# Kernel tuning notes

Measured on AMD Instinct MI355X. Metric: run time of the kernel, lower is better.

Reference implementation:

```python
import jax, jax.numpy as jnp
import numpy as np

BATCH, NSTEPS, IN_F, OUT_F = 8192, 16, 256, 512


def setup_inputs() -> dict:
    key = jax.random.key(0)
    ks = jax.random.split(key, 20)
    r = jax.random.normal
    return {
        "x": r(ks[0], (BATCH, NSTEPS, IN_F), jnp.float32),
        "C": r(ks[1], (BATCH, OUT_F, 1), jnp.float32),
        "H": r(ks[2], (BATCH, OUT_F, 1), jnp.float32),
        "fg_w_c": r(ks[3], (OUT_F, 1), jnp.float32),
        "fg_w_h": r(ks[4], (OUT_F, OUT_F), jnp.float32),
        "fg_w_x": r(ks[5], (OUT_F, IN_F), jnp.float32),
        "fg_b": r(ks[6], (OUT_F, 1), jnp.float32),
        "ig_w_c": r(ks[7], (OUT_F, 1), jnp.float32),
        "ig_w_h": r(ks[8], (OUT_F, OUT_F), jnp.float32),
        "ig_w_x": r(ks[9], (OUT_F, IN_F), jnp.float32),
        "ig_b": r(ks[10], (OUT_F, 1), jnp.float32),
        "in_w_h": r(ks[11], (OUT_F, OUT_F), jnp.float32),
        "in_w_x": r(ks[12], (OUT_F, IN_F), jnp.float32),
        "in_b": r(ks[13], (OUT_F, 1), jnp.float32),
        "og_w_cn": r(ks[14], (OUT_F, 1), jnp.float32),
        "og_w_h": r(ks[15], (OUT_F, OUT_F), jnp.float32),
        "og_w_x": r(ks[16], (OUT_F, IN_F), jnp.float32),
        "og_b": r(ks[17], (OUT_F, 1), jnp.float32),
        "n": 3,
    }


def reference(x, C, H,
              fg_w_c, fg_w_h, fg_w_x, fg_b,
              ig_w_c, ig_w_h, ig_w_x, ig_b,
              in_w_h, in_w_x, in_b,
              og_w_cn, og_w_h, og_w_x, og_b,
              n):
    # x: [B, T, IN] -> current step [B, IN, 1]
    x_cur = x[:, n, :, None]
    # peephole LSTM gates; matmul broadcasts [O,O] @ [B,O,1] -> [B,O,1]
    fg = jax.nn.sigmoid(fg_w_c * C + jnp.matmul(fg_w_h, H) + jnp.matmul(fg_w_x, x_cur) + fg_b)
    ig = jax.nn.sigmoid(ig_w_c * C + jnp.matmul(ig_w_h, H) + jnp.matmul(ig_w_x, x_cur) + ig_b)
    inn = jnp.tanh(jnp.matmul(in_w_h, H) + jnp.matmul(in_w_x, x_cur) + in_b)
    cm = fg * C + ig * inn
    og = jax.nn.sigmoid(og_w_cn * cm + jnp.matmul(og_w_h, H) + jnp.matmul(og_w_x, x_cur) + og_b)
    h = og * jnp.tanh(cm)
    return (cm, h)
```

## Files before the change

### kernel.cpp

```cpp
#include <hip/hip_runtime.h>


typedef _Float16 half8 __attribute__((ext_vector_type(8)));
typedef _Float16 half4v __attribute__((ext_vector_type(4)));
typedef float floatx4 __attribute__((ext_vector_type(4)));

#define BATCH 8192
#define NSTEPS 16
#define IN_F 256
#define OUT_F 512
#define KDIM 768
#define NDIM 2048
#define HSIZE ((size_t)BATCH * OUT_F)

#define BM 128
#define BN 128
#define BK 64

__device__ __forceinline__ void async_copy16(const void* gptr, void* lptr) {
  __builtin_amdgcn_global_load_lds(
      (const __attribute__((address_space(1))) unsigned int*)gptr,
      (__attribute__((address_space(3))) unsigned int*)lptr,
      16, 0, 0);
}

__device__ __forceinline__ float sigmoidf_(float x) {
  return 1.0f / (1.0f + __expf(-x));
}

__device__ __forceinline__ float tanhf_(float x) {
  x = fminf(fmaxf(x, -20.0f), 20.0f);
  float e = __expf(2.0f * x);
  return (e - 1.0f) / (e + 1.0f);
}

__global__ void pack_AW(const float* __restrict__ H, const float* __restrict__ x,
                        const int* __restrict__ nptr,
                        const float* __restrict__ fg_w_h, const float* __restrict__ fg_w_x,
                        const float* __restrict__ ig_w_h, const float* __restrict__ ig_w_x,
                        const float* __restrict__ in_w_h, const float* __restrict__ in_w_x,
                        const float* __restrict__ og_w_h, const float* __restrict__ og_w_x,
                        _Float16* __restrict__ A, _Float16* __restrict__ W) {
  const int blk = blockIdx.x;
  const int k = threadIdx.x * 4;
  const float* src;
  _Float16* dst;
  if (blk < BATCH) {
    const int b = blk;
    if (k < OUT_F) {
      src = H + (size_t)b * OUT_F + k;
    } else {
      const int n = *nptr;
      src = x + ((size_t)b * NSTEPS + n) * IN_F + (k - OUT_F);
    }
    dst = A + (size_t)b * KDIM + k;
  } else {
    const int row = blk - BATCH;
    const int g  = (row >> 4) & 3;
    const int jj = ((row >> 6) << 4) | (row & 15);
    if (k < OUT_F) {
      const float* wh = (g == 0) ? fg_w_h : (g == 1) ? ig_w_h : (g == 2) ? in_w_h : og_w_h;
      src = wh + (size_t)jj * OUT_F + k;
    } else {
      const float* wx = (g == 0) ? fg_w_x : (g == 1) ? ig_w_x : (g == 2) ? in_w_x : og_w_x;
      src = wx + (size_t)jj * IN_F + (k - OUT_F);
    }
    dst = W + (size_t)row * KDIM + k;
  }
  float4 v = *(const float4*)src;
  half4v h = {(_Float16)v.x, (_Float16)v.y, (_Float16)v.z, (_Float16)v.w};
  *(half4v*)dst = h;
}

__global__ __launch_bounds__(256, 4) void gemm_lstm(
    const _Float16* __restrict__ A, const _Float16* __restrict__ W,
    const float* __restrict__ C,
    const float* __restrict__ fg_w_c, const float* __restrict__ fg_b,
    const float* __restrict__ ig_w_c, const float* __restrict__ ig_b,
    const float* __restrict__ in_b,
    const float* __restrict__ og_w_cn, const float* __restrict__ og_b,
    float* __restrict__ out) {
  __shared__ __align__(16) _Float16 As[BM * BK];
  __shared__ __align__(16) _Float16 Bs[BN * BK];

  const int tid = threadIdx.x;
  const int lane = tid & 63;
  const int wave = tid >> 6;
  const int quad = lane >> 4;
  const int l16 = lane & 15;
  const int m0 = blockIdx.y * BM;
  const int n0 = blockIdx.x * BN;
  const int mw = (wave >> 1) * 64;
  const int nw = (wave & 1) * 64;

  const int jj = (((n0 + nw) >> 6) << 4) | l16;
  const float fwc = fg_w_c[jj], fb = fg_b[jj];
  const float iwc = ig_w_c[jj], ib = ig_b[jj];
  const float nb  = in_b[jj];
  const float owc = og_w_cn[jj], ob = og_b[jj];

  floatx4 acc[4][4] = {};

  for (int kt = 0; kt < KDIM; kt += BK) {
    __syncthreads();
#pragma unroll
    for (int r = 0; r < 4; ++r) {
      const int g = r * 256 + tid;
      const int row = g >> 3;
      const int cl = g & 7;
      const int cg = cl ^ (row & 7);
      async_copy16(A + (size_t)(m0 + row) * KDIM + kt + cg * 8,
                   (_Float16*)As + g * 8);
      async_copy16(W + (size_t)(n0 + row) * KDIM + kt + cg * 8,
                   (_Float16*)Bs + g * 8);
    }
    __syncthreads();

#pragma unroll
    for (int ks = 0; ks < 2; ++ks) {
      half8 af[4], bf[4];
#pragma unroll
      for (int i = 0; i < 4; ++i) {
        const int row = mw + i * 16 + l16;
        const int chunk = ks * 4 + quad;
        const int gran = row * 8 + (chunk ^ (row & 7));
        af[i] = *(const half8*)(As + gran * 8);
      }
#pragma unroll
      for (int j = 0; j < 4; ++j) {
        const int row = nw + j * 16 + l16;
        const int chunk = ks * 4 + quad;
        const int gran = row * 8 + (chunk ^ (row & 7));
        bf[j] = *(const half8*)(Bs + gran * 8);
      }
#pragma unroll
      for (int i = 0; i < 4; ++i)
#pragma unroll
        for (int j = 0; j < 4; ++j)
          acc[i][j] = __builtin_amdgcn_mfma_f32_16x16x32_f16(af[i], bf[j], acc[i][j], 0, 0, 0);
    }
  }

  float cv[16];
#pragma unroll
  for (int i = 0; i < 4; ++i) {
    const int rbase = m0 + mw + i * 16 + quad * 4;
#pragma unroll
    for (int r = 0; r < 4; ++r)
      cv[i * 4 + r] = C[(size_t)(rbase + r) * OUT_F + jj];
  }
  float inn[16];
#pragma unroll
  for (int i = 0; i < 4; ++i)
#pragma unroll
    for (int r = 0; r < 4; ++r)
      inn[i * 4 + r] = tanhf_(acc[i][2][r] + nb);
#pragma unroll
  for (int i = 0; i < 4; ++i) {
    const int rbase = m0 + mw + i * 16 + quad * 4;
#pragma unroll
    for (int r = 0; r < 4; ++r) {
      const int b = rbase + r;
      const float c = cv[i * 4 + r];
      const float fg  = sigmoidf_(fwc * c + acc[i][0][r] + fb);
      const float ig  = sigmoidf_(iwc * c + acc[i][1][r] + ib);
      const float cm  = fg * c + ig * inn[i * 4 + r];
      const float og  = sigmoidf_(owc * cm + acc[i][3][r] + ob);
      out[(size_t)b * OUT_F + jj] = cm;
      out[HSIZE + (size_t)b * OUT_F + jj] = og * tanhf_(cm);
    }
  }
}

extern "C" void kernel_launch(void* const* d_in, const int* in_sizes, int n_in,
                              void* d_out, int out_size, void* d_ws, size_t ws_size,
                              hipStream_t stream) {
  const float* x       = (const float*)d_in[0];
  const float* C       = (const float*)d_in[1];
  const float* H       = (const float*)d_in[2];
  const float* fg_w_c  = (const float*)d_in[3];
  const float* fg_w_h  = (const float*)d_in[4];
  const float* fg_w_x  = (const float*)d_in[5];
  const float* fg_b    = (const float*)d_in[6];
  const float* ig_w_c  = (const float*)d_in[7];
  const float* ig_w_h  = (const float*)d_in[8];
  const float* ig_w_x  = (const float*)d_in[9];
  const float* ig_b    = (const float*)d_in[10];
  const float* in_w_h  = (const float*)d_in[11];
  const float* in_w_x  = (const float*)d_in[12];
  const float* in_b    = (const float*)d_in[13];
  const float* og_w_cn = (const float*)d_in[14];
  const float* og_w_h  = (const float*)d_in[15];
  const float* og_w_x  = (const float*)d_in[16];
  const float* og_b    = (const float*)d_in[17];
  const int*   nptr    = (const int*)d_in[18];

  char* ws = (char*)d_ws;
  _Float16* Apk = (_Float16*)ws;
  _Float16* Wpk = (_Float16*)(ws + 12582912);
  (void)ws_size; (void)in_sizes; (void)n_in; (void)out_size;

  pack_AW<<<BATCH + NDIM, 192, 0, stream>>>(H, x, nptr,
                                            fg_w_h, fg_w_x, ig_w_h, ig_w_x,
                                            in_w_h, in_w_x, og_w_h, og_w_x,
                                            Apk, Wpk);
  dim3 grid(NDIM / BN, BATCH / BM);
  gemm_lstm<<<grid, 256, 0, stream>>>(Apk, Wpk, C,
                                      fg_w_c, fg_b, ig_w_c, ig_b, in_b,
                                      og_w_cn, og_b, (float*)d_out);
}
```

Before: 259.2 us.

## Restructure GEMM to stage weights in LDS and stream A rows from global

Replaces the 128x128 tiled GEMM with 1024-thread blocks that each own 64 output columns and 1024 batch rows. A 64-column half-K weight slice is staged in LDS, and each wave reads its A fragments straight from global memory instead of through shared memory. The intent is to cut LDS traffic for A and reuse each weight slice across many rows. The risk is uncoalesced, latency-bound A loads from global memory with no pipelining, and a grid of only 256 blocks.

After: 299.0 us. 1.15x slower.

```diff
diff --git a/kernel.cpp b/kernel.cpp
--- a/kernel.cpp
+++ b/kernel.cpp
@@ -13,9 +13,10 @@
 #define NDIM 2048
 #define HSIZE ((size_t)BATCH * OUT_F)
 
-#define BM 128
-#define BN 128
-#define BK 64
+#define COLS 64
+#define ROWS_BLK 1024
+#define KHALF 384
+#define KC_PASS 48
 
 __device__ __forceinline__ void async_copy16(const void* gptr, void* lptr) {
   __builtin_amdgcn_global_load_lds(
@@ -72,7 +73,7 @@
   *(half4v*)dst = h;
 }
 
-__global__ __launch_bounds__(256, 4) void gemm_lstm(
+__global__ __launch_bounds__(1024, 4) void gemm_lstm(
     const _Float16* __restrict__ A, const _Float16* __restrict__ W,
     const float* __restrict__ C,
     const float* __restrict__ fg_w_c, const float* __restrict__ fg_b,
@@ -80,58 +81,55 @@
     const float* __restrict__ in_b,
     const float* __restrict__ og_w_cn, const float* __restrict__ og_b,
     float* __restrict__ out) {
-  __shared__ __align__(16) _Float16 As[BM * BK];
-  __shared__ __align__(16) _Float16 Bs[BN * BK];
+  __shared__ __align__(16) _Float16 Ws[COLS * KC_PASS * 8];
 
   const int tid = threadIdx.x;
   const int lane = tid & 63;
   const int wave = tid >> 6;
   const int quad = lane >> 4;
   const int l16 = lane & 15;
-  const int m0 = blockIdx.y * BM;
-  const int n0 = blockIdx.x * BN;
-  const int mw = (wave >> 1) * 64;
-  const int nw = (wave & 1) * 64;
-
-  const int jj = (((n0 + nw) >> 6) << 4) | l16;
+
+  const int fid = blockIdx.x;
+  const int rg   = fid & 7;
+  const int colb = fid >> 3;
+  const int n0 = colb * COLS;
+  const int mw = rg * ROWS_BLK + wave * 64;
+
+  const int jj = (colb << 4) | l16;
   const float fwc = fg_w_c[jj], fb = fg_b[jj];
   const float iwc = ig_w_c[jj], ib = ig_b[jj];
   const float nb  = in_b[jj];
   const float owc = og_w_cn[jj], ob = og_b[jj];
 
+  const _Float16* Abase = A + (size_t)mw * KDIM;
+
   floatx4 acc[4][4] = {};
 
-  for (int kt = 0; kt < KDIM; kt += BK) {
+#pragma unroll
+  for (int kh = 0; kh < 2; ++kh) {
     __syncthreads();
 #pragma unroll
-    for (int r = 0; r < 4; ++r) {
-      const int g = r * 256 + tid;
-      const int row = g >> 3;
-      const int cl = g & 7;
-      const int cg = cl ^ (row & 7);
-      async_copy16(A + (size_t)(m0 + row) * KDIM + kt + cg * 8,
-                   (_Float16*)As + g * 8);
-      async_copy16(W + (size_t)(n0 + row) * KDIM + kt + cg * 8,
-                   (_Float16*)Bs + g * 8);
+    for (int it = 0; it < 3; ++it) {
+      const int s = it * 1024 + tid;
+      const int col = s / KC_PASS;
+      const int kc = s - col * KC_PASS;
+      const int kcg = kc ^ (col & 7);
+      async_copy16(W + (size_t)(n0 + col) * KDIM + kh * KHALF + kcg * 8,
+                   (_Float16*)Ws + s * 8);
     }
     __syncthreads();
 
-#pragma unroll
-    for (int ks = 0; ks < 2; ++ks) {
+    for (int ks = 0; ks < 12; ++ks) {
+      const int kbase = kh * KHALF + ks * 32 + quad * 8;
       half8 af[4], bf[4];
 #pragma unroll
-      for (int i = 0; i < 4; ++i) {
-        const int row = mw + i * 16 + l16;
-        const int chunk = ks * 4 + quad;
-        const int gran = row * 8 + (chunk ^ (row & 7));
-        af[i] = *(const half8*)(As + gran * 8);
-      }
+      for (int i = 0; i < 4; ++i)
+        af[i] = *(const half8*)(Abase + (size_t)(i * 16 + l16) * KDIM + kbase);
 #pragma unroll
       for (int j = 0; j < 4; ++j) {
-        const int row = nw + j * 16 + l16;
-        const int chunk = ks * 4 + quad;
-        const int gran = row * 8 + (chunk ^ (row & 7));
-        bf[j] = *(const half8*)(Bs + gran * 8);
+        const int cl = j * 16 + l16;
+        const int kc = (ks * 4 + quad) ^ (cl & 7);
+        bf[j] = *(const half8*)(Ws + (cl * KC_PASS + kc) * 8);
       }
 #pragma unroll
       for (int i = 0; i < 4; ++i)
@@ -144,7 +142,7 @@
   float cv[16];
 #pragma unroll
   for (int i = 0; i < 4; ++i) {
-    const int rbase = m0 + mw + i * 16 + quad * 4;
+    const int rbase = mw + i * 16 + quad * 4;
 #pragma unroll
     for (int r = 0; r < 4; ++r)
       cv[i * 4 + r] = C[(size_t)(rbase + r) * OUT_F + jj];
@@ -157,7 +155,7 @@
       inn[i * 4 + r] = tanhf_(acc[i][2][r] + nb);
 #pragma unroll
   for (int i = 0; i < 4; ++i) {
-    const int rbase = m0 + mw + i * 16 + quad * 4;
+    const int rbase = mw + i * 16 + quad * 4;
 #pragma unroll
     for (int r = 0; r < 4; ++r) {
       const int b = rbase + r;
@@ -204,8 +202,7 @@
                                             fg_w_h, fg_w_x, ig_w_h, ig_w_x,
                                             in_w_h, in_w_x, og_w_h, og_w_x,
                                             Apk, Wpk);
-  dim3 grid(NDIM / BN, BATCH / BM);
-  gemm_lstm<<<grid, 256, 0, stream>>>(Apk, Wpk, C,
+  gemm_lstm<<<256, 1024, 0, stream>>>(Apk, Wpk, C,
                                       fg_w_c, fg_b, ig_w_c, ig_b, in_b,
                                       og_w_cn, og_b, (float*)d_out);
 }
```
